# Performance work log

Measured on AMD Instinct MI355X. Metric: run time of the kernel, lower is better.

Reference implementation:

```python
import jax, jax.numpy as jnp
import numpy as np

# dims
K = 32       # num_particles
B = 32       # batch_size
T = 64       # seq_len
H = 256      # hidden_dim
E_OBS = 128  # emb_obs
E_ACT = 128  # emb_act
OBS_NUM = 64
WIN = 50     # window_length
ALPHA = 0.5  # resamp_alpha
E = E_OBS + E_ACT  # cell input size


def _lin(k, fan_in, fan_out):
    kw, kb = jax.random.split(k)
    lim = 1.0 / np.sqrt(fan_in)
    W = jax.random.uniform(kw, (fan_out, fan_in), minval=-lim, maxval=lim, dtype=jnp.float32)
    b = jax.random.uniform(kb, (fan_out,), minval=-lim, maxval=lim, dtype=jnp.float32)
    return W, b


def setup_inputs() -> dict:
    key = jax.random.key(0)
    ks = jax.random.split(key, 10)
    obs_in = jax.random.normal(ks[0], (B, T, OBS_NUM), dtype=jnp.float32)
    prev_window = jax.random.normal(ks[1], (B, T, WIN), dtype=jnp.float32)
    W_obs, b_obs = _lin(ks[2], OBS_NUM, E_OBS)
    W_act, b_act = _lin(ks[3], WIN, E_ACT)
    W_ih, b_ih = _lin(ks[4], E, 5 * H)
    W_hh, b_hh = _lin(ks[5], H, 5 * H)
    W_fcobs, b_fcobs = _lin(ks[6], H + E, 1)
    W_lab, b_lab = _lin(ks[7], H, 1)
    # init_hidden with initialize == 'rand' (torch.rand -> uniform[0,1))
    h0 = jax.random.uniform(ks[8], (K * B, H), dtype=jnp.float32)
    c0 = jax.random.uniform(ks[9], (K * B, H), dtype=jnp.float32)
    return dict(obs_in=obs_in, prev_window=prev_window, W_obs=W_obs, b_obs=b_obs,
                W_act=W_act, b_act=b_act, W_ih=W_ih, b_ih=b_ih, W_hh=W_hh, b_hh=b_hh,
                W_fcobs=W_fcobs, b_fcobs=b_fcobs, W_lab=W_lab, b_lab=b_lab, h0=h0, c0=c0)


def reference(obs_in, prev_window, W_obs, b_obs, W_act, b_act, W_ih, b_ih,
              W_hh, b_hh, W_fcobs, b_fcobs, W_lab, b_lab, h0, c0):
    # input embeddings
    obs_emb = jax.nn.relu(jnp.einsum('bto,eo->bte', obs_in, W_obs) + b_obs)
    act_emb = jax.nn.relu(jnp.einsum('btw,ew->bte', prev_window, W_act) + b_act)
    emb = jnp.concatenate([obs_emb, act_emb], axis=2)          # [B,T,E]
    emb = jnp.tile(emb, (K, 1, 1))                             # [K*B,T,E] particle-major
    xs = jnp.swapaxes(emb, 0, 1)                               # [T,K*B,E]
    p0 = jnp.full((K * B, 1), np.log(1.0 / K), dtype=jnp.float32)
    step_keys = jax.random.split(jax.random.key(42), T)        # per-step sampling keys
    offset = jnp.arange(B)

    def step(carry, inp):
        h, c, p = carry
        x, kstep = inp
        k_eps, k_res = jax.random.split(kstep)
        # PF-LSTM gates: i, f, g, o + variance head for stochastic cell state
        gates = x @ W_ih.T + b_ih + h @ W_hh.T + b_hh           # [KB,5H]
        i, f, g, o, var = jnp.split(gates, 5, axis=1)
        c1 = jax.nn.sigmoid(f) * c + jax.nn.sigmoid(i) * jnp.tanh(g)
        # reparameterization trick: c1 ~ N(c1, softplus(var)^2)
        c1 = c1 + jax.random.normal(k_eps, c1.shape, c1.dtype) * jax.nn.softplus(var)
        h1 = jax.nn.sigmoid(o) * jnp.tanh(c1)
        # observation likelihood -> particle log-weight update, normalized over particles
        logpdf = jnp.concatenate([h1, x], axis=1) @ W_fcobs.T + b_fcobs  # [KB,1]
        p1 = jax.nn.log_softmax((logpdf + p).reshape(K, B, 1), axis=0).reshape(-1, 1)
        # soft resampling: q = alpha*w + (1-alpha)/K
        rp = ALPHA * jnp.exp(p1) + (1.0 - ALPHA) / K            # [KB,1]
        logits = jnp.log(rp.reshape(K, B).T)                    # [B,K]
        idx = jax.random.categorical(k_res, logits, shape=(K, B))  # [K,B]
        flat = (offset[None, :] + idx * B).reshape(-1)          # [KB]
        h_n = h1[flat]
        c_n = c1[flat]
        # importance weight correction: w' = w / q, renormalized in log space
        pn = jnp.exp(p1.reshape(-1)[flat])
        pn = pn / (ALPHA * pn + (1.0 - ALPHA) / K)
        pn = jnp.log(pn).reshape(K, B, 1)
        pn = (pn - jax.scipy.special.logsumexp(pn, axis=0, keepdims=True)).reshape(-1, 1)
        return (h_n, c_n, pn), (h_n, pn)

    _, (hs, ps) = jax.lax.scan(step, (h0, c0, p0), (xs, step_keys))
    # hs: [T,KB,H], ps: [T,KB,1]; dropout rate is 0.0 -> identity
    w = jnp.exp(ps.reshape(T, K, B, 1))
    y = jnp.sum(hs.reshape(T, K, B, H) * w, axis=1)             # weighted particle mean [T,B,H]
    y_out = jax.nn.sigmoid(y @ W_lab.T + b_lab)                 # [T,B,1]
    pf_out = jax.nn.sigmoid(hs @ W_lab.T + b_lab)               # [T,KB,1]
    return y_out, pf_out
```

## Files before the change

### kernel.cpp

```cpp
#include <hip/hip_runtime.h>
#include <math.h>

#define KP   32
#define BB   32
#define TT   64
#define HH   256
#define KB   1024

__host__ __device__ __forceinline__ unsigned rotl32(unsigned v, int s) {
  return (v << s) | (v >> (32 - s));
}
__host__ __device__ __forceinline__ void tf2x32(unsigned k0, unsigned k1,
                                                unsigned c0, unsigned c1,
                                                unsigned& o0, unsigned& o1) {
  unsigned ks2 = k0 ^ k1 ^ 0x1BD11BDAu;
  unsigned x0 = c0 + k0, x1 = c1 + k1;
#define TF_R4(a,b,c,d)                                           \
  x0 += x1; x1 = rotl32(x1, a); x1 ^= x0;                        \
  x0 += x1; x1 = rotl32(x1, b); x1 ^= x0;                        \
  x0 += x1; x1 = rotl32(x1, c); x1 ^= x0;                        \
  x0 += x1; x1 = rotl32(x1, d); x1 ^= x0;
  TF_R4(13,15,26,6)  x0 += k1;  x1 += ks2 + 1u;
  TF_R4(17,29,16,24) x0 += ks2; x1 += k0 + 2u;
  TF_R4(13,15,26,6)  x0 += k0;  x1 += k1 + 3u;
  TF_R4(17,29,16,24) x0 += k1;  x1 += ks2 + 4u;
  TF_R4(13,15,26,6)  x0 += ks2; x1 += k0 + 5u;
#undef TF_R4
  o0 = x0; o1 = x1;
}
__device__ __forceinline__ unsigned tfx(unsigned k0, unsigned k1, unsigned ctr) {
  unsigned a, b;
  tf2x32(k0, k1, 0u, ctr, a, b);
  return a ^ b;
}

__device__ __forceinline__ float sigf(float x) { return 1.0f / (1.0f + expf(-x)); }

__device__ __forceinline__ float erfinv_f(float x) {
  float w = -log1pf(-x * x);
  float p;
  if (w < 5.0f) {
    w -= 2.5f;
    p = 2.81022636e-08f;
    p = fmaf(p, w, 3.43273939e-07f);
    p = fmaf(p, w, -3.5233877e-06f);
    p = fmaf(p, w, -4.39150654e-06f);
    p = fmaf(p, w, 0.00021858087f);
    p = fmaf(p, w, -0.00125372503f);
    p = fmaf(p, w, -0.00417768164f);
    p = fmaf(p, w, 0.246640727f);
    p = fmaf(p, w, 1.50140941f);
  } else {
    w = sqrtf(w) - 3.0f;
    p = -0.000200214257f;
    p = fmaf(p, w, 0.000100950558f);
    p = fmaf(p, w, 0.00134934322f);
    p = fmaf(p, w, -0.00367342844f);
    p = fmaf(p, w, 0.00573950773f);
    p = fmaf(p, w, -0.0076224613f);
    p = fmaf(p, w, 0.00943887047f);
    p = fmaf(p, w, 1.00167406f);
    p = fmaf(p, w, 2.83297682f);
  }
  return p * x;
}

__device__ __forceinline__ float normal_from_bits(unsigned bits) {
  float u01 = __uint_as_float(0x3f800000u | (bits >> 9)) - 1.0f;
  const float lo = -0.99999994f;
  float u = fmaxf(fmaf(u01, 2.0f, lo), lo);
  return 1.41421354f * erfinv_f(u);
}

__global__ __launch_bounds__(256) void transpose_w_kernel(
    const float* __restrict__ W, float4* __restrict__ Wt4) {
  int idx = blockIdx.x * 256 + threadIdx.x;
  int k4 = idx / 1280, j = idx - k4 * 1280;
  Wt4[idx] = *(const float4*)&W[(size_t)j * 256 + k4 * 4];
}

__global__ __launch_bounds__(256) void emb_kernel(
    const float* __restrict__ obs, const float* __restrict__ win,
    const float* __restrict__ Wobs, const float* __restrict__ bobs,
    const float* __restrict__ Wact, const float* __restrict__ bact,
    float* __restrict__ embT) {
  int r = blockIdx.x;
  int t = r >> 5, b = r & 31;
  __shared__ float xs[64];
  __shared__ float ws[50];
  int tid = threadIdx.x;
  if (tid < 64) xs[tid] = obs[(b * 64 + t) * 64 + tid];
  else if (tid < 114) ws[tid - 64] = win[(b * 64 + t) * 50 + (tid - 64)];
  __syncthreads();
  int e = tid;
  float acc = 0.0f;
  if (e < 128) {
    const float* wr = Wobs + e * 64;
    for (int o = 0; o < 64; ++o) acc = fmaf(xs[o], wr[o], acc);
    acc += bobs[e];
  } else {
    int e2 = e - 128;
    const float* wr = Wact + e2 * 50;
    for (int o = 0; o < 50; ++o) acc = fmaf(ws[o], wr[o], acc);
    acc += bact[e2];
  }
  embT[r * 256 + e] = fmaxf(acc, 0.0f);
}

__global__ __launch_bounds__(256) void xdot_kernel(
    const float* __restrict__ embT, const float* __restrict__ Wf,
    const float* __restrict__ bf, float* __restrict__ xdot) {
  int wave = threadIdx.x >> 6, lane = threadIdx.x & 63;
  int r = blockIdx.x * 4 + wave;
  const float4* row = (const float4*)(embT + (size_t)r * 256);
  const float4* wv  = (const float4*)(Wf + 256);
  float4 a = row[lane];
  float4 w = wv[lane];
  float s = a.x * w.x + a.y * w.y + a.z * w.z + a.w * w.w;
  for (int m = 1; m < 64; m <<= 1) s += __shfl_xor(s, m);
  if (lane == 0) xdot[r] = s + bf[0];
}

__global__ __launch_bounds__(512, 4) void xw_kernel(
    const float* __restrict__ embT, const float4* __restrict__ Wt4ih,
    const float* __restrict__ bih, const float* __restrict__ bhh,
    float* __restrict__ xw) {
  int cg = blockIdx.x & 7;
  int rt = blockIdx.x >> 3;
  __shared__ float As[32 * 256];
  int tid = threadIdx.x;
  {
    const float4* src = (const float4*)(embT + (size_t)rt * 32 * 256);
    float4* dst = (float4*)As;
    for (int i = tid; i < 32 * 64; i += 512) dst[i] = src[i];
  }
  __syncthreads();
  int rg = tid >> 5, hcol = tid & 31;
  int jh = cg * 32 + hcol;
  float acc[2][5] = {};
  #pragma unroll 2
  for (int k4 = 0; k4 < 64; ++k4) {
    float4 hv[2], wv[5];
    #pragma unroll
    for (int i = 0; i < 2; ++i)
      hv[i] = *(const float4*)&As[(rg * 2 + i) * 256 + k4 * 4];
    #pragma unroll
    for (int g = 0; g < 5; ++g)
      wv[g] = Wt4ih[k4 * 1280 + g * 256 + jh];
    #pragma unroll
    for (int i = 0; i < 2; ++i)
      #pragma unroll
      for (int g = 0; g < 5; ++g) {
        acc[i][g] = fmaf(hv[i].x, wv[g].x, acc[i][g]);
        acc[i][g] = fmaf(hv[i].y, wv[g].y, acc[i][g]);
        acc[i][g] = fmaf(hv[i].z, wv[g].z, acc[i][g]);
        acc[i][g] = fmaf(hv[i].w, wv[g].w, acc[i][g]);
      }
  }
  for (int i = 0; i < 2; ++i) {
    int r = rt * 32 + rg * 2 + i;
    for (int g = 0; g < 5; ++g) {
      int j = g * 256 + jh;
      xw[(size_t)r * 1280 + j] = acc[i][g] + bih[j] + bhh[j];
    }
  }
}

__global__ __launch_bounds__(512, 2) void step_kernel(
    int t, unsigned ke0, unsigned ke1, unsigned kr0, unsigned kr1,
    const float* __restrict__ h_prev, const float* __restrict__ c_prev,
    float* __restrict__ h_next, float* __restrict__ c_next,
    const float* __restrict__ parts_prev, float* __restrict__ parts_cur,
    const float* __restrict__ labparts_prev, float* __restrict__ labparts_cur,
    const float* __restrict__ ps_prev, float* __restrict__ ps_out,
    float* __restrict__ lab_out, float* __restrict__ pf_out,
    const float* __restrict__ xdot, const float* __restrict__ xw,
    const float4* __restrict__ Wt4hh, const float* __restrict__ Wf,
    const float* __restrict__ Wlab, const float* __restrict__ blab) {
  const int tid = threadIdx.x;
  const int cg = blockIdx.x & 7;
  const int rt = blockIdx.x >> 3;

  __shared__ float sarr[1024];
  __shared__ float mtab[32], ltab[32];
  __shared__ int   flat_s[32];
  __shared__ float h_s[32 * 256];

  if (t == 0) {
    if (tid < 32) flat_s[tid] = rt * 32 + tid;
  } else {
    for (int idx = tid; idx < 1024; idx += 512) {
      float lp = 0.0f;
      #pragma unroll
      for (int c2 = 0; c2 < 8; ++c2) lp += parts_prev[c2 * 1024 + idx];
      lp += xdot[(t - 1) * 32 + (idx & 31)];
      float pp = ps_prev ? ps_prev[idx] : -3.4657359f;
      sarr[idx] = lp + pp;
    }
    __syncthreads();
    if (tid < 32) {
      const int b = tid;
      float m = -INFINITY;
      for (int k = 0; k < 32; ++k) m = fmaxf(m, sarr[k * 32 + b]);
      float s = 0.0f;
      for (int k = 0; k < 32; ++k) s += expf(sarr[k * 32 + b] - m);
      mtab[b] = m; ltab[b] = logf(s);
    }
    __syncthreads();
    {
      const int q = tid >> 4, s16 = tid & 15;
      const float m = mtab[q], l = ltab[q];
      float best = -INFINITY; int bestj = 0;
      for (int jj = 0; jj < 2; ++jj) {
        int j = s16 * 2 + jj;
        unsigned bits = tfx(kr0, kr1, (unsigned)(rt * 1024 + q * 32 + j));
        float u01 = __uint_as_float(0x3f800000u | (bits >> 9)) - 1.0f;
        float u = fmaxf(u01, 1.17549435e-38f);
        float g = -logf(-logf(u));
        float p1 = sarr[j * 32 + q] - m - l;
        float z = g + logf(fmaf(0.5f, expf(p1), 0.015625f));
        if (z > best) { best = z; bestj = j; }
      }
      #pragma unroll
      for (int mm = 1; mm < 16; mm <<= 1) {
        float ob = __shfl_xor(best, mm);
        int   oj = __shfl_xor(bestj, mm);
        if (ob > best || (ob == best && oj < bestj)) { best = ob; bestj = oj; }
      }
      if (s16 == 0) {
        int fl = bestj * 32 + q;
        flat_s[q] = fl;
        if (cg == 0) {
          float p1f = sarr[fl] - m - l;
          float e = expf(p1f);
          ps_out[rt * 32 + q] = logf(e / fmaf(0.5f, e, 0.015625f));
        }
      }
    }
    if (cg == 0) {
      __syncthreads();
      if (tid < 32) {
        int fl = flat_s[tid];
        float lab = 0.0f;
        #pragma unroll
        for (int c2 = 0; c2 < 8; ++c2) lab += labparts_prev[c2 * 1024 + fl];
        lab_out[rt * 32 + tid] = lab;
        float v = lab + blab[0];
        pf_out[rt * 32 + tid] = 1.0f / (1.0f + expf(-v));
      }
    }
  }
  __syncthreads();
  if (t >= 64) return;

  {
    float4* dst = (float4*)h_s;
    for (int i = tid; i < 32 * 64; i += 512) {
      int rr = i >> 6, kc = i & 63;
      dst[i] = *(const float4*)(h_prev + (size_t)flat_s[rr] * 256 + kc * 4);
    }
  }
  __syncthreads();

  const int rg = tid >> 5, hcol = tid & 31;
  const int jh = cg * 32 + hcol;
  float acc[2][5] = {};
  #pragma unroll 4
  for (int k4 = 0; k4 < 64; ++k4) {
    float4 hv[2], wv[5];
    #pragma unroll
    for (int i = 0; i < 2; ++i)
      hv[i] = *(const float4*)&h_s[(rg * 2 + i) * 256 + k4 * 4];
    #pragma unroll
    for (int g = 0; g < 5; ++g)
      wv[g] = Wt4hh[k4 * 1280 + g * 256 + jh];
    #pragma unroll
    for (int i = 0; i < 2; ++i)
      #pragma unroll
      for (int g = 0; g < 5; ++g) {
        acc[i][g] = fmaf(hv[i].x, wv[g].x, acc[i][g]);
        acc[i][g] = fmaf(hv[i].y, wv[g].y, acc[i][g]);
        acc[i][g] = fmaf(hv[i].z, wv[g].z, acc[i][g]);
        acc[i][g] = fmaf(hv[i].w, wv[g].w, acc[i][g]);
      }
  }

  const float wfj = Wf[jh];
  const float wlj = Wlab[jh];
  #pragma unroll
  for (int i = 0; i < 2; ++i) {
    const int rl = rg * 2 + i;
    const int kb = rt * 32 + rl;
    const float* xr = xw + (size_t)(t * 32 + rl) * 1280;
    float gi = acc[i][0] + xr[jh];
    float gf = acc[i][1] + xr[256 + jh];
    float gg = acc[i][2] + xr[512 + jh];
    float go = acc[i][3] + xr[768 + jh];
    float gv = acc[i][4] + xr[1024 + jh];
    float cp = c_prev[(size_t)flat_s[rl] * 256 + jh];
    float c1 = sigf(gf) * cp + sigf(gi) * tanhf(gg);
    unsigned bits = tfx(ke0, ke1, (unsigned)(kb * 256 + jh));
    float z = normal_from_bits(bits);
    float sp = fmaxf(gv, 0.0f) + log1pf(expf(-fabsf(gv)));
    c1 = c1 + z * sp;
    float h1 = sigf(go) * tanhf(c1);
    h_next[(size_t)kb * 256 + jh] = h1;
    c_next[(size_t)kb * 256 + jh] = c1;
    float ph = h1 * wfj, pb = h1 * wlj;
    #pragma unroll
    for (int mm = 1; mm < 32; mm <<= 1) {
      ph += __shfl_xor(ph, mm);
      pb += __shfl_xor(pb, mm);
    }
    if (hcol == 0) {
      parts_cur[cg * 1024 + kb] = ph;
      labparts_cur[cg * 1024 + kb] = pb;
    }
  }
}

__global__ __launch_bounds__(256) void final_kernel(
    const float* __restrict__ ps_store, const float* __restrict__ lab_full,
    const float* __restrict__ blab, float* __restrict__ yout) {
  int idx = blockIdx.x * 256 + threadIdx.x;
  if (idx >= 2048) return;
  int t = idx >> 5, b = idx & 31;
  const float* pl = ps_store + (size_t)t * 1024 + b;
  const float* lb = lab_full + (size_t)t * 1024 + b;
  float m = -INFINITY;
  for (int k = 0; k < 32; ++k) m = fmaxf(m, pl[k * 32]);
  float num = 0.0f, den = 0.0f;
  for (int k = 0; k < 32; ++k) {
    float w = expf(pl[k * 32] - m);
    num += w * lb[k * 32];
    den += w;
  }
  float y = num / den;
  yout[idx] = 1.0f / (1.0f + expf(-(y + blab[0])));
}

extern "C" void kernel_launch(void* const* d_in, const int* in_sizes, int n_in,
                              void* d_out, int out_size, void* d_ws,
                              size_t ws_size, hipStream_t stream) {
  const float* obs  = (const float*)d_in[0];
  const float* win  = (const float*)d_in[1];
  const float* Wobs = (const float*)d_in[2];
  const float* bobs = (const float*)d_in[3];
  const float* Wact = (const float*)d_in[4];
  const float* bact = (const float*)d_in[5];
  const float* Wih  = (const float*)d_in[6];
  const float* bih  = (const float*)d_in[7];
  const float* Whh  = (const float*)d_in[8];
  const float* bhh  = (const float*)d_in[9];
  const float* Wf   = (const float*)d_in[10];
  const float* bf   = (const float*)d_in[11];
  const float* Wlab = (const float*)d_in[12];
  const float* blab = (const float*)d_in[13];
  const float* h0   = (const float*)d_in[14];
  const float* c0   = (const float*)d_in[15];
  float* out = (float*)d_out;

  char* ws = (char*)d_ws;
  float* embT = (float*)ws;                 ws += (size_t)2048 * 256 * 4;
  float* xw   = (float*)ws;                 ws += (size_t)2048 * 1280 * 4;
  float* xd   = (float*)ws;                 ws += (size_t)2048 * 4;
  float* hbuf[2]; float* cbuf[2];
  hbuf[0] = (float*)ws;                     ws += (size_t)1024 * 256 * 4;
  hbuf[1] = (float*)ws;                     ws += (size_t)1024 * 256 * 4;
  cbuf[0] = (float*)ws;                     ws += (size_t)1024 * 256 * 4;
  cbuf[1] = (float*)ws;                     ws += (size_t)1024 * 256 * 4;
  float* parts    = (float*)ws;             ws += (size_t)2 * 8 * 1024 * 4;
  float* labparts = (float*)ws;             ws += (size_t)2 * 8 * 1024 * 4;
  float* psst     = (float*)ws;             ws += (size_t)64 * 1024 * 4;
  float* labf     = (float*)ws;             ws += (size_t)64 * 1024 * 4;

  float4* Wt4ih = (float4*)hbuf[1];
  float4* Wt4hh = (float4*)embT;

  transpose_w_kernel<<<320, 256, 0, stream>>>(Wih, Wt4ih);
  emb_kernel<<<2048, 256, 0, stream>>>(obs, win, Wobs, bobs, Wact, bact, embT);
  xw_kernel<<<512, 512, 0, stream>>>(embT, Wt4ih, bih, bhh, xw);
  xdot_kernel<<<512, 256, 0, stream>>>(embT, Wf, bf, xd);
  transpose_w_kernel<<<320, 256, 0, stream>>>(Whh, Wt4hh);

  for (int t = 0; t <= 64; ++t) {
    unsigned a0, a1, ke0 = 0, ke1 = 0, kr0 = 0, kr1 = 0;
    if (t < 64) {
      tf2x32(0u, 42u, 0u, (unsigned)t, a0, a1);
      tf2x32(a0, a1, 0u, 0u, ke0, ke1);
    }
    if (t >= 1) {
      tf2x32(0u, 42u, 0u, (unsigned)(t - 1), a0, a1);
      tf2x32(a0, a1, 0u, 1u, kr0, kr1);
    }
    const float* hp = (t == 0) ? h0 : hbuf[(t - 1) & 1];
    const float* cp = (t == 0) ? c0 : cbuf[(t - 1) & 1];
    float* hn = hbuf[t & 1];
    float* cn = cbuf[t & 1];
    const float* pprev = (t >= 2) ? psst + (size_t)(t - 2) * 1024 : nullptr;
    int tm1 = (t >= 1) ? (t - 1) : 0;
    step_kernel<<<256, 512, 0, stream>>>(
        t, ke0, ke1, kr0, kr1, hp, cp, hn, cn,
        parts + (size_t)((t + 1) & 1) * 8192, parts + (size_t)(t & 1) * 8192,
        labparts + (size_t)((t + 1) & 1) * 8192,
        labparts + (size_t)(t & 1) * 8192,
        pprev, psst + (size_t)tm1 * 1024, labf + (size_t)tm1 * 1024,
        out + 2048 + (size_t)tm1 * 1024,
        xd, xw, Wt4hh, Wf, Wlab, blab);
  }

  final_kernel<<<8, 256, 0, stream>>>(psst, labf, blab, out);
  (void)in_sizes; (void)n_in; (void)out_size; (void)ws_size;
}
```

Before: 2.156 ms.

## Split gate columns across 16 blocks of 256 threads and double-buffer loads

The step and xw kernels now use 256-thread blocks, each owning 16 hidden columns instead of 32, so the grids double (512 and 1024 blocks). The partial-sum buffers for the fc and label projections widen from 8 to 16 column groups, and the resampling logic is rebalanced to 8 lanes per batch element. The inner matvec loop also prefetches the next k-slice of weights and hidden state before doing the FMAs. The goal is more blocks to fill the GPU and better hiding of load latency. The cost is that every block redundantly does the per-step resampling prologue and gathers the full h tile, so that duplicated work doubles.

After: 2.296 ms. 6.5% more time.

```diff
diff --git a/kernel.cpp b/kernel.cpp
--- a/kernel.cpp
+++ b/kernel.cpp
@@ -121,41 +121,56 @@
   if (lane == 0) xdot[r] = s + bf[0];
 }
 
-__global__ __launch_bounds__(512, 4) void xw_kernel(
+#define LOADW(dst, k4v)                                                   \
+  {                                                                       \
+    _Pragma("unroll")                                                     \
+    for (int g = 0; g < 5; ++g) dst[g] = wbase[(k4v) * 1280 + g * 256];   \
+  }
+#define LOADH(h0v, h1v, k4v)                                              \
+  h0v = *(const float4*)&h_s[(rg * 2 + 0) * 256 + (k4v) * 4];             \
+  h1v = *(const float4*)&h_s[(rg * 2 + 1) * 256 + (k4v) * 4];
+#define FMA5(hv0, hv1, wv)                                                \
+  {                                                                       \
+    _Pragma("unroll")                                                     \
+    for (int g = 0; g < 5; ++g) {                                         \
+      acc[0][g] = fmaf(hv0.x, wv[g].x, acc[0][g]);                        \
+      acc[0][g] = fmaf(hv0.y, wv[g].y, acc[0][g]);                        \
+      acc[0][g] = fmaf(hv0.z, wv[g].z, acc[0][g]);                        \
+      acc[0][g] = fmaf(hv0.w, wv[g].w, acc[0][g]);                        \
+      acc[1][g] = fmaf(hv1.x, wv[g].x, acc[1][g]);                        \
+      acc[1][g] = fmaf(hv1.y, wv[g].y, acc[1][g]);                        \
+      acc[1][g] = fmaf(hv1.z, wv[g].z, acc[1][g]);                        \
+      acc[1][g] = fmaf(hv1.w, wv[g].w, acc[1][g]);                        \
+    }                                                                     \
+  }
+
+__global__ __launch_bounds__(256, 4) void xw_kernel(
     const float* __restrict__ embT, const float4* __restrict__ Wt4ih,
     const float* __restrict__ bih, const float* __restrict__ bhh,
     float* __restrict__ xw) {
-  int cg = blockIdx.x & 7;
-  int rt = blockIdx.x >> 3;
-  __shared__ float As[32 * 256];
+  int cg = blockIdx.x & 15;
+  int rt = blockIdx.x >> 4;
+  __shared__ float h_s[32 * 256];
   int tid = threadIdx.x;
   {
     const float4* src = (const float4*)(embT + (size_t)rt * 32 * 256);
-    float4* dst = (float4*)As;
-    for (int i = tid; i < 32 * 64; i += 512) dst[i] = src[i];
+    float4* dst = (float4*)h_s;
+    for (int i = tid; i < 32 * 64; i += 256) dst[i] = src[i];
   }
   __syncthreads();
-  int rg = tid >> 5, hcol = tid & 31;
-  int jh = cg * 32 + hcol;
+  int rg = tid >> 4, hcol = tid & 15;
+  int jh = cg * 16 + hcol;
+  const float4* wbase = Wt4ih + jh;
   float acc[2][5] = {};
+  float4 wva[5], wvb[5], ha0, ha1, hb0, hb1;
+  LOADW(wva, 0) LOADH(ha0, ha1, 0)
   #pragma unroll 2
-  for (int k4 = 0; k4 < 64; ++k4) {
-    float4 hv[2], wv[5];
-    #pragma unroll
-    for (int i = 0; i < 2; ++i)
-      hv[i] = *(const float4*)&As[(rg * 2 + i) * 256 + k4 * 4];
-    #pragma unroll
-    for (int g = 0; g < 5; ++g)
-      wv[g] = Wt4ih[k4 * 1280 + g * 256 + jh];
-    #pragma unroll
-    for (int i = 0; i < 2; ++i)
-      #pragma unroll
-      for (int g = 0; g < 5; ++g) {
-        acc[i][g] = fmaf(hv[i].x, wv[g].x, acc[i][g]);
-        acc[i][g] = fmaf(hv[i].y, wv[g].y, acc[i][g]);
-        acc[i][g] = fmaf(hv[i].z, wv[g].z, acc[i][g]);
-        acc[i][g] = fmaf(hv[i].w, wv[g].w, acc[i][g]);
-      }
+  for (int k4 = 0; k4 < 64; k4 += 2) {
+    LOADW(wvb, k4 + 1) LOADH(hb0, hb1, k4 + 1)
+    FMA5(ha0, ha1, wva)
+    int k4n = (k4 + 2) & 63;
+    LOADW(wva, k4n) LOADH(ha0, ha1, k4n)
+    FMA5(hb0, hb1, wvb)
   }
   for (int i = 0; i < 2; ++i) {
     int r = rt * 32 + rg * 2 + i;
@@ -166,7 +181,7 @@
   }
 }
 
-__global__ __launch_bounds__(512, 2) void step_kernel(
+__global__ __launch_bounds__(256, 2) void step_kernel(
     int t, unsigned ke0, unsigned ke1, unsigned kr0, unsigned kr1,
     const float* __restrict__ h_prev, const float* __restrict__ c_prev,
     float* __restrict__ h_next, float* __restrict__ c_next,
@@ -178,8 +193,8 @@
     const float4* __restrict__ Wt4hh, const float* __restrict__ Wf,
     const float* __restrict__ Wlab, const float* __restrict__ blab) {
   const int tid = threadIdx.x;
-  const int cg = blockIdx.x & 7;
-  const int rt = blockIdx.x >> 3;
+  const int cg = blockIdx.x & 15;
+  const int rt = blockIdx.x >> 4;
 
   __shared__ float sarr[1024];
   __shared__ float mtab[32], ltab[32];
@@ -189,10 +204,10 @@
   if (t == 0) {
     if (tid < 32) flat_s[tid] = rt * 32 + tid;
   } else {
-    for (int idx = tid; idx < 1024; idx += 512) {
+    for (int idx = tid; idx < 1024; idx += 256) {
       float lp = 0.0f;
       #pragma unroll
-      for (int c2 = 0; c2 < 8; ++c2) lp += parts_prev[c2 * 1024 + idx];
+      for (int c2 = 0; c2 < 16; ++c2) lp += parts_prev[c2 * 1024 + idx];
       lp += xdot[(t - 1) * 32 + (idx & 31)];
       float pp = ps_prev ? ps_prev[idx] : -3.4657359f;
       sarr[idx] = lp + pp;
@@ -208,11 +223,11 @@
     }
     __syncthreads();
     {
-      const int q = tid >> 4, s16 = tid & 15;
+      const int q = tid >> 3, s8 = tid & 7;
       const float m = mtab[q], l = ltab[q];
       float best = -INFINITY; int bestj = 0;
-      for (int jj = 0; jj < 2; ++jj) {
-        int j = s16 * 2 + jj;
+      for (int jj = 0; jj < 4; ++jj) {
+        int j = s8 * 4 + jj;
         unsigned bits = tfx(kr0, kr1, (unsigned)(rt * 1024 + q * 32 + j));
         float u01 = __uint_as_float(0x3f800000u | (bits >> 9)) - 1.0f;
         float u = fmaxf(u01, 1.17549435e-38f);
@@ -222,12 +237,12 @@
         if (z > best) { best = z; bestj = j; }
       }
       #pragma unroll
-      for (int mm = 1; mm < 16; mm <<= 1) {
+      for (int mm = 1; mm < 8; mm <<= 1) {
         float ob = __shfl_xor(best, mm);
         int   oj = __shfl_xor(bestj, mm);
         if (ob > best || (ob == best && oj < bestj)) { best = ob; bestj = oj; }
       }
-      if (s16 == 0) {
+      if (s8 == 0) {
         int fl = bestj * 32 + q;
         flat_s[q] = fl;
         if (cg == 0) {
@@ -243,7 +258,7 @@
         int fl = flat_s[tid];
         float lab = 0.0f;
         #pragma unroll
-        for (int c2 = 0; c2 < 8; ++c2) lab += labparts_prev[c2 * 1024 + fl];
+        for (int c2 = 0; c2 < 16; ++c2) lab += labparts_prev[c2 * 1024 + fl];
         lab_out[rt * 32 + tid] = lab;
         float v = lab + blab[0];
         pf_out[rt * 32 + tid] = 1.0f / (1.0f + expf(-v));
@@ -255,34 +270,26 @@
 
   {
     float4* dst = (float4*)h_s;
-    for (int i = tid; i < 32 * 64; i += 512) {
+    for (int i = tid; i < 32 * 64; i += 256) {
       int rr = i >> 6, kc = i & 63;
       dst[i] = *(const float4*)(h_prev + (size_t)flat_s[rr] * 256 + kc * 4);
     }
   }
   __syncthreads();
 
-  const int rg = tid >> 5, hcol = tid & 31;
-  const int jh = cg * 32 + hcol;
+  const int rg = tid >> 4, hcol = tid & 15;
+  const int jh = cg * 16 + hcol;
+  const float4* wbase = Wt4hh + jh;
   float acc[2][5] = {};
-  #pragma unroll 4
-  for (int k4 = 0; k4 < 64; ++k4) {
-    float4 hv[2], wv[5];
-    #pragma unroll
-    for (int i = 0; i < 2; ++i)
-      hv[i] = *(const float4*)&h_s[(rg * 2 + i) * 256 + k4 * 4];
-    #pragma unroll
-    for (int g = 0; g < 5; ++g)
-      wv[g] = Wt4hh[k4 * 1280 + g * 256 + jh];
-    #pragma unroll
-    for (int i = 0; i < 2; ++i)
-      #pragma unroll
-      for (int g = 0; g < 5; ++g) {
-        acc[i][g] = fmaf(hv[i].x, wv[g].x, acc[i][g]);
-        acc[i][g] = fmaf(hv[i].y, wv[g].y, acc[i][g]);
-        acc[i][g] = fmaf(hv[i].z, wv[g].z, acc[i][g]);
-        acc[i][g] = fmaf(hv[i].w, wv[g].w, acc[i][g]);
-      }
+  float4 wva[5], wvb[5], ha0, ha1, hb0, hb1;
+  LOADW(wva, 0) LOADH(ha0, ha1, 0)
+  #pragma unroll 2
+  for (int k4 = 0; k4 < 64; k4 += 2) {
+    LOADW(wvb, k4 + 1) LOADH(hb0, hb1, k4 + 1)
+    FMA5(ha0, ha1, wva)
+    int k4n = (k4 + 2) & 63;
+    LOADW(wva, k4n) LOADH(ha0, ha1, k4n)
+    FMA5(hb0, hb1, wvb)
   }
 
   const float wfj = Wf[jh];
@@ -308,7 +315,7 @@
     c_next[(size_t)kb * 256 + jh] = c1;
     float ph = h1 * wfj, pb = h1 * wlj;
     #pragma unroll
-    for (int mm = 1; mm < 32; mm <<= 1) {
+    for (int mm = 1; mm < 16; mm <<= 1) {
       ph += __shfl_xor(ph, mm);
       pb += __shfl_xor(pb, mm);
     }
@@ -369,8 +376,8 @@
   hbuf[1] = (float*)ws;                     ws += (size_t)1024 * 256 * 4;
   cbuf[0] = (float*)ws;                     ws += (size_t)1024 * 256 * 4;
   cbuf[1] = (float*)ws;                     ws += (size_t)1024 * 256 * 4;
-  float* parts    = (float*)ws;             ws += (size_t)2 * 8 * 1024 * 4;
-  float* labparts = (float*)ws;             ws += (size_t)2 * 8 * 1024 * 4;
+  float* parts    = (float*)ws;             ws += (size_t)2 * 16 * 1024 * 4;
+  float* labparts = (float*)ws;             ws += (size_t)2 * 16 * 1024 * 4;
   float* psst     = (float*)ws;             ws += (size_t)64 * 1024 * 4;
   float* labf     = (float*)ws;             ws += (size_t)64 * 1024 * 4;
 
@@ -379,7 +386,7 @@
 
   transpose_w_kernel<<<320, 256, 0, stream>>>(Wih, Wt4ih);
   emb_kernel<<<2048, 256, 0, stream>>>(obs, win, Wobs, bobs, Wact, bact, embT);
-  xw_kernel<<<512, 512, 0, stream>>>(embT, Wt4ih, bih, bhh, xw);
+  xw_kernel<<<1024, 256, 0, stream>>>(embT, Wt4ih, bih, bhh, xw);
   xdot_kernel<<<512, 256, 0, stream>>>(embT, Wf, bf, xd);
   transpose_w_kernel<<<320, 256, 0, stream>>>(Whh, Wt4hh);
 
@@ -399,11 +406,11 @@
     float* cn = cbuf[t & 1];
     const float* pprev = (t >= 2) ? psst + (size_t)(t - 2) * 1024 : nullptr;
     int tm1 = (t >= 1) ? (t - 1) : 0;
-    step_kernel<<<256, 512, 0, stream>>>(
+    step_kernel<<<512, 256, 0, stream>>>(
         t, ke0, ke1, kr0, kr1, hp, cp, hn, cn,
-        parts + (size_t)((t + 1) & 1) * 8192, parts + (size_t)(t & 1) * 8192,
-        labparts + (size_t)((t + 1) & 1) * 8192,
-        labparts + (size_t)(t & 1) * 8192,
+        parts + (size_t)((t + 1) & 1) * 16384, parts + (size_t)(t & 1) * 16384,
+        labparts + (size_t)((t + 1) & 1) * 16384,
+        labparts + (size_t)(t & 1) * 16384,
         pprev, psst + (size_t)tm1 * 1024, labf + (size_t)tm1 * 1024,
         out + 2048 + (size_t)tm1 * 1024,
         xd, xw, Wt4hh, Wf, Wlab, blab);
```

## Fuse per-step launches into a persistent kernel with grid barriers and LDS-resident weights

Applied to the files above, without the earlier changes.

Replaces the 65 per-timestep step_kernel launches with a single persistent kernel of 256 blocks that synchronises through an atomic grid barrier. Each block now keeps its 16-column slice of the transposed W_hh in shared memory for all steps and handles 64 rows, using a padded h tile. The goal is to remove launch overhead and the repeated global reads of W_hh on every step. The risks are deadlock if the 256 blocks are not all co-resident (the launch bounds give 2 blocks per CU), higher LDS pressure, and the cost of spin-wait barriers.

Measured after the change: 3.738 ms. 73.4% more time.

```diff
diff --git a/kernel.cpp b/kernel.cpp
--- a/kernel.cpp
+++ b/kernel.cpp
@@ -6,6 +6,7 @@
 #define TT   64
 #define HH   256
 #define KB   1024
+#define HPAD 260
 
 __host__ __device__ __forceinline__ unsigned rotl32(unsigned v, int s) {
   return (v << s) | (v >> (32 - s));
@@ -72,6 +73,27 @@
   return 1.41421354f * erfinv_f(u);
 }
 
+__device__ __forceinline__ void grid_barrier(unsigned* bar, unsigned tgt) {
+  __syncthreads();
+  if (threadIdx.x == 0) {
+    __threadfence();
+    unsigned old = __hip_atomic_fetch_add(bar, 1u, __ATOMIC_ACQ_REL,
+                                          __HIP_MEMORY_SCOPE_AGENT);
+    if (old == 255u) {
+      __hip_atomic_store(bar, 0u, __ATOMIC_RELAXED, __HIP_MEMORY_SCOPE_AGENT);
+      __hip_atomic_fetch_add(bar + 1, 1u, __ATOMIC_RELEASE,
+                             __HIP_MEMORY_SCOPE_AGENT);
+    } else {
+      while (__hip_atomic_load(bar + 1, __ATOMIC_ACQUIRE,
+                               __HIP_MEMORY_SCOPE_AGENT) < tgt) {
+        __builtin_amdgcn_s_sleep(2);
+      }
+    }
+    __threadfence();
+  }
+  __syncthreads();
+}
+
 __global__ __launch_bounds__(256) void transpose_w_kernel(
     const float* __restrict__ W, float4* __restrict__ Wt4) {
   int idx = blockIdx.x * 256 + threadIdx.x;
@@ -138,7 +160,7 @@
   int rg = tid >> 5, hcol = tid & 31;
   int jh = cg * 32 + hcol;
   float acc[2][5] = {};
-  #pragma unroll 2
+  #pragma unroll 4
   for (int k4 = 0; k4 < 64; ++k4) {
     float4 hv[2], wv[5];
     #pragma unroll
@@ -166,35 +188,204 @@
   }
 }
 
-__global__ __launch_bounds__(512, 2) void step_kernel(
-    int t, unsigned ke0, unsigned ke1, unsigned kr0, unsigned kr1,
-    const float* __restrict__ h_prev, const float* __restrict__ c_prev,
-    float* __restrict__ h_next, float* __restrict__ c_next,
-    const float* __restrict__ parts_prev, float* __restrict__ parts_cur,
-    const float* __restrict__ labparts_prev, float* __restrict__ labparts_cur,
-    const float* __restrict__ ps_prev, float* __restrict__ ps_out,
-    float* __restrict__ lab_out, float* __restrict__ pf_out,
+__global__ __launch_bounds__(512, 2) void pf_persist(
+    unsigned* __restrict__ bar,
+    const float* __restrict__ h0, const float* __restrict__ c0,
+    float* __restrict__ hbuf, float* __restrict__ cbuf,
+    float* __restrict__ parts, float* __restrict__ labparts,
+    float* __restrict__ psst, float* __restrict__ labf,
+    float* __restrict__ pf_out,
     const float* __restrict__ xdot, const float* __restrict__ xw,
     const float4* __restrict__ Wt4hh, const float* __restrict__ Wf,
     const float* __restrict__ Wlab, const float* __restrict__ blab) {
   const int tid = threadIdx.x;
-  const int cg = blockIdx.x & 7;
-  const int rt = blockIdx.x >> 3;
-
-  __shared__ float sarr[1024];
-  __shared__ float mtab[32], ltab[32];
-  __shared__ int   flat_s[32];
-  __shared__ float h_s[32 * 256];
-
-  if (t == 0) {
-    if (tid < 32) flat_s[tid] = rt * 32 + tid;
-  } else {
+  const int cg = blockIdx.x & 15;
+  const int pt = blockIdx.x >> 4;
+
+  __shared__ float4 w_s[64 * 5 * 16];
+  __shared__ float  h_s[64 * HPAD];
+  __shared__ float  sarr[1024];
+  __shared__ float  mtab[32], ltab[32];
+  __shared__ int    flat_s[64];
+
+  for (int i = tid; i < 5120; i += 512) {
+    int k4 = i / 80, r = i - k4 * 80;
+    w_s[i] = Wt4hh[k4 * 1280 + (r >> 4) * 256 + cg * 16 + (r & 15)];
+  }
+
+  const int rg = tid >> 4, hcol = tid & 15;
+  const int jh = cg * 16 + hcol;
+  const float wfj = Wf[jh];
+  const float wlj = Wlab[jh];
+  const float blab0 = blab[0];
+
+  for (int t = 0; t < 64; ++t) {
+    if (t == 0) {
+      if (tid < 64) flat_s[tid] = pt * 64 + tid;
+    } else {
+      grid_barrier(bar, (unsigned)t);
+      const int tres = t - 1;
+      const float* pprev = parts + (size_t)(tres & 1) * 16384;
+      for (int idx = tid; idx < 1024; idx += 512) {
+        const float4* pr = (const float4*)(pprev + (size_t)idx * 16);
+        float4 p0 = pr[0], p1 = pr[1], p2 = pr[2], p3 = pr[3];
+        float lp = 0.0f;
+        lp += p0.x; lp += p0.y; lp += p0.z; lp += p0.w;
+        lp += p1.x; lp += p1.y; lp += p1.z; lp += p1.w;
+        lp += p2.x; lp += p2.y; lp += p2.z; lp += p2.w;
+        lp += p3.x; lp += p3.y; lp += p3.z; lp += p3.w;
+        lp += xdot[tres * 32 + (idx & 31)];
+        float pp = tres ? psst[(size_t)(tres - 1) * 1024 + idx] : -3.4657359f;
+        sarr[idx] = lp + pp;
+      }
+      __syncthreads();
+      if (tid < 32) {
+        const int b = tid;
+        float m = -INFINITY;
+        for (int k = 0; k < 32; ++k) m = fmaxf(m, sarr[k * 32 + b]);
+        float s = 0.0f;
+        for (int k = 0; k < 32; ++k) s += expf(sarr[k * 32 + b] - m);
+        mtab[b] = m; ltab[b] = logf(s);
+      }
+      __syncthreads();
+      {
+        unsigned a0, a1, kr0, kr1;
+        tf2x32(0u, 42u, 0u, (unsigned)tres, a0, a1);
+        tf2x32(a0, a1, 0u, 1u, kr0, kr1);
+        const int lr = tid >> 3, s8 = tid & 7;
+        const int u = lr >> 5, q = lr & 31;
+        const int kpar = pt * 2 + u;
+        const float m = mtab[q], l = ltab[q];
+        float best = -INFINITY; int bestj = 0;
+        for (int jj = 0; jj < 4; ++jj) {
+          int j = s8 * 4 + jj;
+          unsigned bits = tfx(kr0, kr1, (unsigned)(kpar * 1024 + q * 32 + j));
+          float u01 = __uint_as_float(0x3f800000u | (bits >> 9)) - 1.0f;
+          float uu = fmaxf(u01, 1.17549435e-38f);
+          float g = -logf(-logf(uu));
+          float p1 = sarr[j * 32 + q] - m - l;
+          float z = g + logf(fmaf(0.5f, expf(p1), 0.015625f));
+          if (z > best) { best = z; bestj = j; }
+        }
+        #pragma unroll
+        for (int mm = 1; mm < 8; mm <<= 1) {
+          float ob = __shfl_xor(best, mm);
+          int   oj = __shfl_xor(bestj, mm);
+          if (ob > best || (ob == best && oj < bestj)) { best = ob; bestj = oj; }
+        }
+        if (s8 == 0) {
+          int fl = bestj * 32 + q;
+          flat_s[lr] = fl;
+          if (cg == 0) {
+            float p1f = sarr[fl] - m - l;
+            float e = expf(p1f);
+            psst[(size_t)tres * 1024 + pt * 64 + lr] =
+                logf(e / fmaf(0.5f, e, 0.015625f));
+          }
+        }
+      }
+      if (cg == 0) {
+        __syncthreads();
+        if (tid < 64) {
+          int fl = flat_s[tid];
+          const float* lpp = labparts + (size_t)(tres & 1) * 16384 +
+                             (size_t)fl * 16;
+          float lab = 0.0f;
+          #pragma unroll
+          for (int c2 = 0; c2 < 16; ++c2) lab += lpp[c2];
+          labf[(size_t)tres * 1024 + pt * 64 + tid] = lab;
+          float v = lab + blab0;
+          pf_out[(size_t)tres * 1024 + pt * 64 + tid] =
+              1.0f / (1.0f + expf(-v));
+        }
+      }
+    }
+    __syncthreads();
+
+    const float* hp = (t == 0) ? h0 : hbuf + (size_t)((t - 1) & 1) * 262144;
+    const float* cp = (t == 0) ? c0 : cbuf + (size_t)((t - 1) & 1) * 262144;
+    for (int i = tid; i < 64 * 64; i += 512) {
+      int rr = i >> 6, kc = i & 63;
+      *(float4*)&h_s[rr * HPAD + kc * 4] =
+          *(const float4*)(hp + (size_t)flat_s[rr] * 256 + kc * 4);
+    }
+    __syncthreads();
+
+    float acc[2][5] = {};
+    #pragma unroll 4
+    for (int k4 = 0; k4 < 64; ++k4) {
+      float4 hv[2], wv[5];
+      #pragma unroll
+      for (int i = 0; i < 2; ++i)
+        hv[i] = *(const float4*)&h_s[(rg * 2 + i) * HPAD + k4 * 4];
+      #pragma unroll
+      for (int g = 0; g < 5; ++g)
+        wv[g] = w_s[k4 * 80 + g * 16 + hcol];
+      #pragma unroll
+      for (int i = 0; i < 2; ++i)
+        #pragma unroll
+        for (int g = 0; g < 5; ++g) {
+          acc[i][g] = fmaf(hv[i].x, wv[g].x, acc[i][g]);
+          acc[i][g] = fmaf(hv[i].y, wv[g].y, acc[i][g]);
+          acc[i][g] = fmaf(hv[i].z, wv[g].z, acc[i][g]);
+          acc[i][g] = fmaf(hv[i].w, wv[g].w, acc[i][g]);
+        }
+    }
+
+    unsigned a0, a1, ke0, ke1;
+    tf2x32(0u, 42u, 0u, (unsigned)t, a0, a1);
+    tf2x32(a0, a1, 0u, 0u, ke0, ke1);
+    float* hn = hbuf + (size_t)(t & 1) * 262144;
+    float* cn = cbuf + (size_t)(t & 1) * 262144;
+    float* pc = parts + (size_t)(t & 1) * 16384;
+    float* lc = labparts + (size_t)(t & 1) * 16384;
+    #pragma unroll
+    for (int i = 0; i < 2; ++i) {
+      const int lr = rg * 2 + i;
+      const int kb = pt * 64 + lr;
+      const int b = lr & 31;
+      const float* xr = xw + (size_t)(t * 32 + b) * 1280;
+      float gi = acc[i][0] + xr[jh];
+      float gf = acc[i][1] + xr[256 + jh];
+      float gg = acc[i][2] + xr[512 + jh];
+      float go = acc[i][3] + xr[768 + jh];
+      float gv = acc[i][4] + xr[1024 + jh];
+      float cpv = cp[(size_t)flat_s[lr] * 256 + jh];
+      float c1 = sigf(gf) * cpv + sigf(gi) * tanhf(gg);
+      unsigned bits = tfx(ke0, ke1, (unsigned)(kb * 256 + jh));
+      float z = normal_from_bits(bits);
+      float sp = fmaxf(gv, 0.0f) + log1pf(expf(-fabsf(gv)));
+      c1 = c1 + z * sp;
+      float h1 = sigf(go) * tanhf(c1);
+      hn[(size_t)kb * 256 + jh] = h1;
+      cn[(size_t)kb * 256 + jh] = c1;
+      float ph = h1 * wfj, pb = h1 * wlj;
+      #pragma unroll
+      for (int mm = 1; mm < 16; mm <<= 1) {
+        ph += __shfl_xor(ph, mm);
+        pb += __shfl_xor(pb, mm);
+      }
+      if (hcol == 0) {
+        pc[(size_t)kb * 16 + cg] = ph;
+        lc[(size_t)kb * 16 + cg] = pb;
+      }
+    }
+  }
+
+  grid_barrier(bar, 64u);
+  {
+    const int tres = 63;
+    const float* pprev = parts + (size_t)(tres & 1) * 16384;
     for (int idx = tid; idx < 1024; idx += 512) {
+      const float4* pr = (const float4*)(pprev + (size_t)idx * 16);
+      float4 p0 = pr[0], p1 = pr[1], p2 = pr[2], p3 = pr[3];
       float lp = 0.0f;
-      #pragma unroll
-      for (int c2 = 0; c2 < 8; ++c2) lp += parts_prev[c2 * 1024 + idx];
-      lp += xdot[(t - 1) * 32 + (idx & 31)];
-      float pp = ps_prev ? ps_prev[idx] : -3.4657359f;
+      lp += p0.x; lp += p0.y; lp += p0.z; lp += p0.w;
+      lp += p1.x; lp += p1.y; lp += p1.z; lp += p1.w;
+      lp += p2.x; lp += p2.y; lp += p2.z; lp += p2.w;
+      lp += p3.x; lp += p3.y; lp += p3.z; lp += p3.w;
+      lp += xdot[tres * 32 + (idx & 31)];
+      float pp = psst[(size_t)(tres - 1) * 1024 + idx];
       sarr[idx] = lp + pp;
     }
     __syncthreads();
@@ -208,113 +399,55 @@
     }
     __syncthreads();
     {
-      const int q = tid >> 4, s16 = tid & 15;
+      unsigned a0, a1, kr0, kr1;
+      tf2x32(0u, 42u, 0u, (unsigned)tres, a0, a1);
+      tf2x32(a0, a1, 0u, 1u, kr0, kr1);
+      const int lr = tid >> 3, s8 = tid & 7;
+      const int u = lr >> 5, q = lr & 31;
+      const int kpar = pt * 2 + u;
       const float m = mtab[q], l = ltab[q];
       float best = -INFINITY; int bestj = 0;
-      for (int jj = 0; jj < 2; ++jj) {
-        int j = s16 * 2 + jj;
-        unsigned bits = tfx(kr0, kr1, (unsigned)(rt * 1024 + q * 32 + j));
+      for (int jj = 0; jj < 4; ++jj) {
+        int j = s8 * 4 + jj;
+        unsigned bits = tfx(kr0, kr1, (unsigned)(kpar * 1024 + q * 32 + j));
         float u01 = __uint_as_float(0x3f800000u | (bits >> 9)) - 1.0f;
-        float u = fmaxf(u01, 1.17549435e-38f);
-        float g = -logf(-logf(u));
+        float uu = fmaxf(u01, 1.17549435e-38f);
+        float g = -logf(-logf(uu));
         float p1 = sarr[j * 32 + q] - m - l;
         float z = g + logf(fmaf(0.5f, expf(p1), 0.015625f));
         if (z > best) { best = z; bestj = j; }
       }
       #pragma unroll
-      for (int mm = 1; mm < 16; mm <<= 1) {
+      for (int mm = 1; mm < 8; mm <<= 1) {
         float ob = __shfl_xor(best, mm);
         int   oj = __shfl_xor(bestj, mm);
         if (ob > best || (ob == best && oj < bestj)) { best = ob; bestj = oj; }
       }
-      if (s16 == 0) {
+      if (s8 == 0) {
         int fl = bestj * 32 + q;
-        flat_s[q] = fl;
+        flat_s[lr] = fl;
         if (cg == 0) {
           float p1f = sarr[fl] - m - l;
           float e = expf(p1f);
-          ps_out[rt * 32 + q] = logf(e / fmaf(0.5f, e, 0.015625f));
+          psst[(size_t)tres * 1024 + pt * 64 + lr] =
+              logf(e / fmaf(0.5f, e, 0.015625f));
         }
       }
     }
     if (cg == 0) {
       __syncthreads();
-      if (tid < 32) {
+      if (tid < 64) {
         int fl = flat_s[tid];
+        const float* lpp = labparts + (size_t)(tres & 1) * 16384 +
+                           (size_t)fl * 16;
         float lab = 0.0f;
         #pragma unroll
-        for (int c2 = 0; c2 < 8; ++c2) lab += labparts_prev[c2 * 1024 + fl];
-        lab_out[rt * 32 + tid] = lab;
-        float v = lab + blab[0];
-        pf_out[rt * 32 + tid] = 1.0f / (1.0f + expf(-v));
-      }
-    }
-  }
-  __syncthreads();
-  if (t >= 64) return;
-
-  {
-    float4* dst = (float4*)h_s;
-    for (int i = tid; i < 32 * 64; i += 512) {
-      int rr = i >> 6, kc = i & 63;
-      dst[i] = *(const float4*)(h_prev + (size_t)flat_s[rr] * 256 + kc * 4);
-    }
-  }
-  __syncthreads();
-
-  const int rg = tid >> 5, hcol = tid & 31;
-  const int jh = cg * 32 + hcol;
-  float acc[2][5] = {};
-  #pragma unroll 4
-  for (int k4 = 0; k4 < 64; ++k4) {
-    float4 hv[2], wv[5];
-    #pragma unroll
-    for (int i = 0; i < 2; ++i)
-      hv[i] = *(const float4*)&h_s[(rg * 2 + i) * 256 + k4 * 4];
-    #pragma unroll
-    for (int g = 0; g < 5; ++g)
-      wv[g] = Wt4hh[k4 * 1280 + g * 256 + jh];
-    #pragma unroll
-    for (int i = 0; i < 2; ++i)
-      #pragma unroll
-      for (int g = 0; g < 5; ++g) {
-        acc[i][g] = fmaf(hv[i].x, wv[g].x, acc[i][g]);
-        acc[i][g] = fmaf(hv[i].y, wv[g].y, acc[i][g]);
-        acc[i][g] = fmaf(hv[i].z, wv[g].z, acc[i][g]);
-        acc[i][g] = fmaf(hv[i].w, wv[g].w, acc[i][g]);
-      }
-  }
-
-  const float wfj = Wf[jh];
-  const float wlj = Wlab[jh];
-  #pragma unroll
-  for (int i = 0; i < 2; ++i) {
-    const int rl = rg * 2 + i;
-    const int kb = rt * 32 + rl;
-    const float* xr = xw + (size_t)(t * 32 + rl) * 1280;
-    float gi = acc[i][0] + xr[jh];
-    float gf = acc[i][1] + xr[256 + jh];
-    float gg = acc[i][2] + xr[512 + jh];
-    float go = acc[i][3] + xr[768 + jh];
-    float gv = acc[i][4] + xr[1024 + jh];
-    float cp = c_prev[(size_t)flat_s[rl] * 256 + jh];
-    float c1 = sigf(gf) * cp + sigf(gi) * tanhf(gg);
-    unsigned bits = tfx(ke0, ke1, (unsigned)(kb * 256 + jh));
-    float z = normal_from_bits(bits);
-    float sp = fmaxf(gv, 0.0f) + log1pf(expf(-fabsf(gv)));
-    c1 = c1 + z * sp;
-    float h1 = sigf(go) * tanhf(c1);
-    h_next[(size_t)kb * 256 + jh] = h1;
-    c_next[(size_t)kb * 256 + jh] = c1;
-    float ph = h1 * wfj, pb = h1 * wlj;
-    #pragma unroll
-    for (int mm = 1; mm < 32; mm <<= 1) {
-      ph += __shfl_xor(ph, mm);
-      pb += __shfl_xor(pb, mm);
-    }
-    if (hcol == 0) {
-      parts_cur[cg * 1024 + kb] = ph;
-      labparts_cur[cg * 1024 + kb] = pb;
+        for (int c2 = 0; c2 < 16; ++c2) lab += lpp[c2];
+        labf[(size_t)tres * 1024 + pt * 64 + tid] = lab;
+        float v = lab + blab0;
+        pf_out[(size_t)tres * 1024 + pt * 64 + tid] =
+            1.0f / (1.0f + expf(-v));
+      }
     }
   }
 }
@@ -364,50 +497,27 @@
   float* embT = (float*)ws;                 ws += (size_t)2048 * 256 * 4;
   float* xw   = (float*)ws;                 ws += (size_t)2048 * 1280 * 4;
   float* xd   = (float*)ws;                 ws += (size_t)2048 * 4;
-  float* hbuf[2]; float* cbuf[2];
-  hbuf[0] = (float*)ws;                     ws += (size_t)1024 * 256 * 4;
-  hbuf[1] = (float*)ws;                     ws += (size_t)1024 * 256 * 4;
-  cbuf[0] = (float*)ws;                     ws += (size_t)1024 * 256 * 4;
-  cbuf[1] = (float*)ws;                     ws += (size_t)1024 * 256 * 4;
-  float* parts    = (float*)ws;             ws += (size_t)2 * 8 * 1024 * 4;
-  float* labparts = (float*)ws;             ws += (size_t)2 * 8 * 1024 * 4;
+  float* hbuf = (float*)ws;                 ws += (size_t)2 * 1024 * 256 * 4;
+  float* cbuf = (float*)ws;                 ws += (size_t)2 * 1024 * 256 * 4;
+  float* parts    = (float*)ws;             ws += (size_t)2 * 16 * 1024 * 4;
+  float* labparts = (float*)ws;             ws += (size_t)2 * 16 * 1024 * 4;
   float* psst     = (float*)ws;             ws += (size_t)64 * 1024 * 4;
   float* labf     = (float*)ws;             ws += (size_t)64 * 1024 * 4;
-
-  float4* Wt4ih = (float4*)hbuf[1];
+  unsigned* bar   = (unsigned*)ws;          ws += 64;
+
+  float4* Wt4ih = (float4*)(hbuf + 262144);
   float4* Wt4hh = (float4*)embT;
 
+  hipMemsetAsync(bar, 0, 8, stream);
   transpose_w_kernel<<<320, 256, 0, stream>>>(Wih, Wt4ih);
   emb_kernel<<<2048, 256, 0, stream>>>(obs, win, Wobs, bobs, Wact, bact, embT);
   xw_kernel<<<512, 512, 0, stream>>>(embT, Wt4ih, bih, bhh, xw);
   xdot_kernel<<<512, 256, 0, stream>>>(embT, Wf, bf, xd);
   transpose_w_kernel<<<320, 256, 0, stream>>>(Whh, Wt4hh);
 
-  for (int t = 0; t <= 64; ++t) {
-    unsigned a0, a1, ke0 = 0, ke1 = 0, kr0 = 0, kr1 = 0;
-    if (t < 64) {
-      tf2x32(0u, 42u, 0u, (unsigned)t, a0, a1);
-      tf2x32(a0, a1, 0u, 0u, ke0, ke1);
-    }
-    if (t >= 1) {
-      tf2x32(0u, 42u, 0u, (unsigned)(t - 1), a0, a1);
-      tf2x32(a0, a1, 0u, 1u, kr0, kr1);
-    }
-    const float* hp = (t == 0) ? h0 : hbuf[(t - 1) & 1];
-    const float* cp = (t == 0) ? c0 : cbuf[(t - 1) & 1];
-    float* hn = hbuf[t & 1];
-    float* cn = cbuf[t & 1];
-    const float* pprev = (t >= 2) ? psst + (size_t)(t - 2) * 1024 : nullptr;
-    int tm1 = (t >= 1) ? (t - 1) : 0;
-    step_kernel<<<256, 512, 0, stream>>>(
-        t, ke0, ke1, kr0, kr1, hp, cp, hn, cn,
-        parts + (size_t)((t + 1) & 1) * 8192, parts + (size_t)(t & 1) * 8192,
-        labparts + (size_t)((t + 1) & 1) * 8192,
-        labparts + (size_t)(t & 1) * 8192,
-        pprev, psst + (size_t)tm1 * 1024, labf + (size_t)tm1 * 1024,
-        out + 2048 + (size_t)tm1 * 1024,
-        xd, xw, Wt4hh, Wf, Wlab, blab);
-  }
+  pf_persist<<<256, 512, 0, stream>>>(
+      bar, h0, c0, hbuf, cbuf, parts, labparts, psst, labf,
+      out + 2048, xd, xw, Wt4hh, Wf, Wlab, blab);
 
   final_kernel<<<8, 256, 0, stream>>>(psst, labf, blab, out);
   (void)in_sizes; (void)n_in; (void)out_size; (void)ws_size;
```

## Use 1024-thread blocks with one row per thread in step and xw kernels

Applied to the files above, without the earlier changes.

Step kernel blocks grow to 1024 threads, so each thread handles one row instead of two. The resampling argmax now uses one candidate per lane with a 32-wide shuffle reduction, and the shared h tile is padded to 260 floats per row to avoid bank conflicts. The xw kernel also moves to 1024 threads covering 64 rows per block, halving its grid. Each Whh weight load is now reused by only one row instead of two, which doubles weight traffic per FMA in exchange for more parallel threads per step.

New measurement: 3.019 ms. 1.4x slower.

```diff
diff --git a/kernel.cpp b/kernel.cpp
--- a/kernel.cpp
+++ b/kernel.cpp
@@ -6,6 +6,7 @@
 #define TT   64
 #define HH   256
 #define KB   1024
+#define HPAD 260
 
 __host__ __device__ __forceinline__ unsigned rotl32(unsigned v, int s) {
   return (v << s) | (v >> (32 - s));
@@ -121,32 +122,32 @@
   if (lane == 0) xdot[r] = s + bf[0];
 }
 
-__global__ __launch_bounds__(512, 4) void xw_kernel(
+__global__ __launch_bounds__(1024, 4) void xw_kernel(
     const float* __restrict__ embT, const float4* __restrict__ Wt4ih,
     const float* __restrict__ bih, const float* __restrict__ bhh,
     float* __restrict__ xw) {
   int cg = blockIdx.x & 7;
   int rt = blockIdx.x >> 3;
-  __shared__ float As[32 * 256];
+  __shared__ float h_s[64 * 256];
   int tid = threadIdx.x;
   {
-    const float4* src = (const float4*)(embT + (size_t)rt * 32 * 256);
-    float4* dst = (float4*)As;
-    for (int i = tid; i < 32 * 64; i += 512) dst[i] = src[i];
+    const float4* src = (const float4*)(embT + (size_t)rt * 64 * 256);
+    float4* dst = (float4*)h_s;
+    for (int i = tid; i < 64 * 64; i += 1024) dst[i] = src[i];
   }
   __syncthreads();
   int rg = tid >> 5, hcol = tid & 31;
   int jh = cg * 32 + hcol;
+  const float* hb = h_s + rg * 2 * 256;
   float acc[2][5] = {};
-  #pragma unroll 2
+  #pragma unroll 4
   for (int k4 = 0; k4 < 64; ++k4) {
-    float4 hv[2], wv[5];
+    float4 wv[5], hv[2];
+    #pragma unroll
+    for (int g = 0; g < 5; ++g) wv[g] = Wt4ih[k4 * 1280 + g * 256 + jh];
     #pragma unroll
     for (int i = 0; i < 2; ++i)
-      hv[i] = *(const float4*)&As[(rg * 2 + i) * 256 + k4 * 4];
-    #pragma unroll
-    for (int g = 0; g < 5; ++g)
-      wv[g] = Wt4ih[k4 * 1280 + g * 256 + jh];
+      hv[i] = *(const float4*)&hb[i * 256 + k4 * 4];
     #pragma unroll
     for (int i = 0; i < 2; ++i)
       #pragma unroll
@@ -158,7 +159,7 @@
       }
   }
   for (int i = 0; i < 2; ++i) {
-    int r = rt * 32 + rg * 2 + i;
+    int r = rt * 64 + rg * 2 + i;
     for (int g = 0; g < 5; ++g) {
       int j = g * 256 + jh;
       xw[(size_t)r * 1280 + j] = acc[i][g] + bih[j] + bhh[j];
@@ -166,7 +167,7 @@
   }
 }
 
-__global__ __launch_bounds__(512, 2) void step_kernel(
+__global__ __launch_bounds__(1024, 4) void step_kernel(
     int t, unsigned ke0, unsigned ke1, unsigned kr0, unsigned kr1,
     const float* __restrict__ h_prev, const float* __restrict__ c_prev,
     float* __restrict__ h_next, float* __restrict__ c_next,
@@ -184,12 +185,13 @@
   __shared__ float sarr[1024];
   __shared__ float mtab[32], ltab[32];
   __shared__ int   flat_s[32];
-  __shared__ float h_s[32 * 256];
+  __shared__ float h_s[32 * HPAD];
 
   if (t == 0) {
     if (tid < 32) flat_s[tid] = rt * 32 + tid;
   } else {
-    for (int idx = tid; idx < 1024; idx += 512) {
+    {
+      int idx = tid;
       float lp = 0.0f;
       #pragma unroll
       for (int c2 = 0; c2 < 8; ++c2) lp += parts_prev[c2 * 1024 + idx];
@@ -208,26 +210,22 @@
     }
     __syncthreads();
     {
-      const int q = tid >> 4, s16 = tid & 15;
+      const int q = tid >> 5, j = tid & 31;
       const float m = mtab[q], l = ltab[q];
-      float best = -INFINITY; int bestj = 0;
-      for (int jj = 0; jj < 2; ++jj) {
-        int j = s16 * 2 + jj;
-        unsigned bits = tfx(kr0, kr1, (unsigned)(rt * 1024 + q * 32 + j));
-        float u01 = __uint_as_float(0x3f800000u | (bits >> 9)) - 1.0f;
-        float u = fmaxf(u01, 1.17549435e-38f);
-        float g = -logf(-logf(u));
-        float p1 = sarr[j * 32 + q] - m - l;
-        float z = g + logf(fmaf(0.5f, expf(p1), 0.015625f));
-        if (z > best) { best = z; bestj = j; }
-      }
+      unsigned bits = tfx(kr0, kr1, (unsigned)(rt * 1024 + q * 32 + j));
+      float u01 = __uint_as_float(0x3f800000u | (bits >> 9)) - 1.0f;
+      float u = fmaxf(u01, 1.17549435e-38f);
+      float g = -logf(-logf(u));
+      float p1 = sarr[j * 32 + q] - m - l;
+      float best = g + logf(fmaf(0.5f, expf(p1), 0.015625f));
+      int bestj = j;
       #pragma unroll
-      for (int mm = 1; mm < 16; mm <<= 1) {
+      for (int mm = 1; mm < 32; mm <<= 1) {
         float ob = __shfl_xor(best, mm);
         int   oj = __shfl_xor(bestj, mm);
         if (ob > best || (ob == best && oj < bestj)) { best = ob; bestj = oj; }
       }
-      if (s16 == 0) {
+      if (j == 0) {
         int fl = bestj * 32 + q;
         flat_s[q] = fl;
         if (cg == 0) {
@@ -253,50 +251,41 @@
   __syncthreads();
   if (t >= 64) return;
 
-  {
-    float4* dst = (float4*)h_s;
-    for (int i = tid; i < 32 * 64; i += 512) {
-      int rr = i >> 6, kc = i & 63;
-      dst[i] = *(const float4*)(h_prev + (size_t)flat_s[rr] * 256 + kc * 4);
-    }
+  for (int i = tid; i < 32 * 64; i += 1024) {
+    int rr = i >> 6, kc = i & 63;
+    *(float4*)&h_s[rr * HPAD + kc * 4] =
+        *(const float4*)(h_prev + (size_t)flat_s[rr] * 256 + kc * 4);
   }
   __syncthreads();
 
   const int rg = tid >> 5, hcol = tid & 31;
   const int jh = cg * 32 + hcol;
-  float acc[2][5] = {};
+  const float* hb = h_s + rg * HPAD;
+  float acc[5] = {};
   #pragma unroll 4
   for (int k4 = 0; k4 < 64; ++k4) {
-    float4 hv[2], wv[5];
-    #pragma unroll
-    for (int i = 0; i < 2; ++i)
-      hv[i] = *(const float4*)&h_s[(rg * 2 + i) * 256 + k4 * 4];
-    #pragma unroll
-    for (int g = 0; g < 5; ++g)
-      wv[g] = Wt4hh[k4 * 1280 + g * 256 + jh];
-    #pragma unroll
-    for (int i = 0; i < 2; ++i)
-      #pragma unroll
-      for (int g = 0; g < 5; ++g) {
-        acc[i][g] = fmaf(hv[i].x, wv[g].x, acc[i][g]);
-        acc[i][g] = fmaf(hv[i].y, wv[g].y, acc[i][g]);
-        acc[i][g] = fmaf(hv[i].z, wv[g].z, acc[i][g]);
-        acc[i][g] = fmaf(hv[i].w, wv[g].w, acc[i][g]);
-      }
-  }
-
-  const float wfj = Wf[jh];
-  const float wlj = Wlab[jh];
-  #pragma unroll
-  for (int i = 0; i < 2; ++i) {
-    const int rl = rg * 2 + i;
+    float4 wv[5];
+    #pragma unroll
+    for (int g = 0; g < 5; ++g) wv[g] = Wt4hh[k4 * 1280 + g * 256 + jh];
+    float4 hv = *(const float4*)&hb[k4 * 4];
+    #pragma unroll
+    for (int g = 0; g < 5; ++g) {
+      acc[g] = fmaf(hv.x, wv[g].x, acc[g]);
+      acc[g] = fmaf(hv.y, wv[g].y, acc[g]);
+      acc[g] = fmaf(hv.z, wv[g].z, acc[g]);
+      acc[g] = fmaf(hv.w, wv[g].w, acc[g]);
+    }
+  }
+
+  {
+    const int rl = rg;
     const int kb = rt * 32 + rl;
     const float* xr = xw + (size_t)(t * 32 + rl) * 1280;
-    float gi = acc[i][0] + xr[jh];
-    float gf = acc[i][1] + xr[256 + jh];
-    float gg = acc[i][2] + xr[512 + jh];
-    float go = acc[i][3] + xr[768 + jh];
-    float gv = acc[i][4] + xr[1024 + jh];
+    float gi = acc[0] + xr[jh];
+    float gf = acc[1] + xr[256 + jh];
+    float gg = acc[2] + xr[512 + jh];
+    float go = acc[3] + xr[768 + jh];
+    float gv = acc[4] + xr[1024 + jh];
     float cp = c_prev[(size_t)flat_s[rl] * 256 + jh];
     float c1 = sigf(gf) * cp + sigf(gi) * tanhf(gg);
     unsigned bits = tfx(ke0, ke1, (unsigned)(kb * 256 + jh));
@@ -306,7 +295,7 @@
     float h1 = sigf(go) * tanhf(c1);
     h_next[(size_t)kb * 256 + jh] = h1;
     c_next[(size_t)kb * 256 + jh] = c1;
-    float ph = h1 * wfj, pb = h1 * wlj;
+    float ph = h1 * Wf[jh], pb = h1 * Wlab[jh];
     #pragma unroll
     for (int mm = 1; mm < 32; mm <<= 1) {
       ph += __shfl_xor(ph, mm);
@@ -379,7 +368,7 @@
 
   transpose_w_kernel<<<320, 256, 0, stream>>>(Wih, Wt4ih);
   emb_kernel<<<2048, 256, 0, stream>>>(obs, win, Wobs, bobs, Wact, bact, embT);
-  xw_kernel<<<512, 512, 0, stream>>>(embT, Wt4ih, bih, bhh, xw);
+  xw_kernel<<<256, 1024, 0, stream>>>(embT, Wt4ih, bih, bhh, xw);
   xdot_kernel<<<512, 256, 0, stream>>>(embT, Wf, bf, xd);
   transpose_w_kernel<<<320, 256, 0, stream>>>(Whh, Wt4hh);
 
@@ -399,7 +388,7 @@
     float* cn = cbuf[t & 1];
     const float* pprev = (t >= 2) ? psst + (size_t)(t - 2) * 1024 : nullptr;
     int tm1 = (t >= 1) ? (t - 1) : 0;
-    step_kernel<<<256, 512, 0, stream>>>(
+    step_kernel<<<256, 1024, 0, stream>>>(
         t, ke0, ke1, kr0, kr1, hp, cp, hn, cn,
         parts + (size_t)((t + 1) & 1) * 8192, parts + (size_t)(t & 1) * 8192,
         labparts + (size_t)((t + 1) & 1) * 8192,
```
